# Optimization experiments

Measured on AMD Instinct MI355X. Metric: run time of the kernel, lower is better.

The kernel has to match this reference:

```python
import jax, jax.numpy as jnp
import numpy as np

THRESHOLD = 0.05   # area-ratio cutoff for 'small target'
SMOOTH = 1e-5      # dice smoothing
FG_FRAC = 0.02     # fraction of foreground pixels in synthetic target (< THRESHOLD)


def setup_inputs() -> dict:
    key = jax.random.key(0)
    k1, k2 = jax.random.split(key)
    B, C, H, W = 64, 1, 512, 512
    pred = jax.random.normal(k1, (B, C, H, W), dtype=jnp.float32)
    # sparse binary mask so area_ratio < threshold for (nearly) all samples
    target = (jax.random.uniform(k2, (B, C, H, W)) < FG_FRAC).astype(jnp.float32)
    return {"pred": pred, "target": target}


def reference(pred, target):
    B = pred.shape[0]
    x = pred.reshape(B, -1)    # [B, P] logits
    t = target.reshape(B, -1)  # [B, P] targets in {0,1}

    # per-sample area ratio and validity mask (replaces the Python branch)
    area_ratio = jnp.mean((t > 0.5).astype(jnp.float32), axis=1)  # [B]
    valid = area_ratio < THRESHOLD                                 # [B] bool

    # BCEWithLogits (numerically stable), weighted by clamp(1 + 10*t, max=20)
    bce = jnp.maximum(x, 0.0) - x * t + jnp.log1p(jnp.exp(-jnp.abs(x)))
    pos_weight = jnp.minimum(1.0 + 10.0 * t, 20.0)
    weighted_bce = jnp.mean(bce * pos_weight, axis=1)  # [B]

    # per-sample dice loss
    p = jax.nn.sigmoid(x)
    intersection = jnp.sum(p * t, axis=1)              # [B]
    union = jnp.sum(p, axis=1) + jnp.sum(t, axis=1)    # [B]
    dice_loss = 1.0 - (2.0 * intersection + SMOOTH) / (union + SMOOTH)

    sample_loss = 0.6 * weighted_bce + 0.4 * dice_loss  # [B]

    n_valid = jnp.sum(valid.astype(jnp.float32))
    total = jnp.sum(jnp.where(valid, sample_loss, 0.0))
    return jnp.where(n_valid > 0, total / jnp.maximum(n_valid, 1.0), 0.0)
```

## Files before the change

### kernel.cpp

```cpp
#include <hip/hip_runtime.h>


#define B_SAMPLES 64
#define P_ELEMS   262144
#define P4        (P_ELEMS / 4)
#define BPS       32
#define TPB       256
#define CHUNK4    (P4 / BPS)
#define ITERS     (CHUNK4 / TPB)

__global__ __launch_bounds__(TPB) void stal_partial(
        const float* __restrict__ pred,
        const float* __restrict__ target,
        float* __restrict__ ws) {
    const int blk    = blockIdx.x;
    const int sample = blk >> 5;
    const int bin    = blk & (BPS - 1);
    const int tid    = threadIdx.x;

    const float4* p4 = reinterpret_cast<const float4*>(pred)
                       + (size_t)sample * P4 + (size_t)bin * CHUNK4;
    const float4* t4 = reinterpret_cast<const float4*>(target)
                       + (size_t)sample * P4 + (size_t)bin * CHUNK4;

    float s_bce = 0.f, s_pt = 0.f, s_p = 0.f, s_t = 0.f;

    #pragma unroll
    for (int i = 0; i < ITERS; ++i) {
        float4 xv = p4[tid + i * TPB];
        float4 tv = t4[tid + i * TPB];
        #pragma unroll
        for (int j = 0; j < 4; ++j) {
            float x = (&xv.x)[j];
            float t = (&tv.x)[j];
            float ax = fabsf(x);
            float e  = __expf(-ax);
            float r  = __builtin_amdgcn_rcpf(1.f + e);
            float p  = (x >= 0.f) ? r : 1.f - r;
            float bce = fmaxf(x, 0.f) - x * t + __logf(1.f + e);
            s_bce = fmaf(bce, fmaf(10.f, t, 1.f), s_bce);
            s_p  += p;
            s_pt  = fmaf(p, t, s_pt);
            s_t  += t;
        }
    }

    for (int off = 32; off > 0; off >>= 1) {
        s_bce += __shfl_down(s_bce, off);
        s_pt  += __shfl_down(s_pt,  off);
        s_p   += __shfl_down(s_p,   off);
        s_t   += __shfl_down(s_t,   off);
    }

    __shared__ float red[4][4];
    const int wave = tid >> 6;
    const int lane = tid & 63;
    if (lane == 0) {
        red[wave][0] = s_bce; red[wave][1] = s_pt;
        red[wave][2] = s_p;   red[wave][3] = s_t;
    }
    __syncthreads();
    if (tid == 0) {
        float a = 0.f, b = 0.f, c = 0.f, d = 0.f;
        for (int w = 0; w < 4; ++w) {
            a += red[w][0]; b += red[w][1]; c += red[w][2]; d += red[w][3];
        }
        float* o = ws + (size_t)blk * 4;
        o[0] = a; o[1] = b; o[2] = c; o[3] = d;
    }
}

__global__ __launch_bounds__(64) void stal_finalize(
        const float* __restrict__ ws,
        float* __restrict__ out) {
    const int b = threadIdx.x;

    float S0 = 0.f, S1 = 0.f, S2 = 0.f, S3 = 0.f;
    for (int k = 0; k < BPS; ++k) {
        const float* o = ws + ((size_t)b * BPS + k) * 4;
        S0 += o[0]; S1 += o[1]; S2 += o[2]; S3 += o[3];
    }

    const float invP = 1.f / (float)P_ELEMS;
    float area   = S3 * invP;
    bool  valid  = area < 0.05f;
    float wbce   = S0 * invP;
    float dice   = 1.f - (2.f * S1 + 1e-5f) / (S2 + S3 + 1e-5f);
    float loss   = 0.6f * wbce + 0.4f * dice;

    float v       = valid ? 1.f : 0.f;
    float contrib = valid ? loss : 0.f;
    for (int off = 32; off > 0; off >>= 1) {
        contrib += __shfl_down(contrib, off);
        v       += __shfl_down(v, off);
    }
    if (b == 0) {
        out[0] = (v > 0.f) ? contrib / fmaxf(v, 1.f) : 0.f;
    }
}

extern "C" void kernel_launch(void* const* d_in, const int* in_sizes, int n_in,
                              void* d_out, int out_size, void* d_ws, size_t ws_size,
                              hipStream_t stream) {
    const float* pred   = (const float*)d_in[0];
    const float* target = (const float*)d_in[1];
    float* out = (float*)d_out;
    float* ws  = (float*)d_ws;

    stal_partial <<<B_SAMPLES * BPS, TPB, 0, stream>>>(pred, target, ws);
    stal_finalize<<<1, 64, 0, stream>>>(ws, out);
}
```

Before: 29.24 us.

## Fuse finalize into partial kernel via last-block atomic and simplify BCE math

Merges the two-kernel reduction into one kernel: each block bumps an atomic counter after writing its partials, and the last block to arrive performs the per-sample finalize and the cross-sample mean. The per-element math is also rewritten to use log(1+exp(x)) with an exp2/log2 pair, and the x*t term is pulled out into a separate accumulator, which removes the abs, select and max operations. A memset is added to reset the counter on every call. Because log2(1+exp(x)) is computed without the stable abs form, it can overflow for large positive logits.

Result: slower. 94.66 us (+223.8%).

```diff
diff --git a/kernel.cpp b/kernel.cpp
--- a/kernel.cpp
+++ b/kernel.cpp
@@ -5,14 +5,20 @@
 #define P_ELEMS   262144
 #define P4        (P_ELEMS / 4)
 #define BPS       32
+#define NBLK      (B_SAMPLES * BPS)
 #define TPB       256
 #define CHUNK4    (P4 / BPS)
 #define ITERS     (CHUNK4 / TPB)
 
-__global__ __launch_bounds__(TPB) void stal_partial(
+#define LOG2E 1.44269504088896340736f
+#define LN2   0.69314718055994530942f
+
+__global__ __launch_bounds__(TPB) void stal_fused(
         const float* __restrict__ pred,
         const float* __restrict__ target,
-        float* __restrict__ ws) {
+        float* __restrict__ ws,
+        unsigned int* __restrict__ counter,
+        float* __restrict__ out) {
     const int blk    = blockIdx.x;
     const int sample = blk >> 5;
     const int bin    = blk & (BPS - 1);
@@ -23,7 +29,7 @@
     const float4* t4 = reinterpret_cast<const float4*>(target)
                        + (size_t)sample * P4 + (size_t)bin * CHUNK4;
 
-    float s_bce = 0.f, s_pt = 0.f, s_p = 0.f, s_t = 0.f;
+    float s_l2w = 0.f, s_xt = 0.f, s_p = 0.f, s_pt = 0.f, s_t = 0.f;
 
     #pragma unroll
     for (int i = 0; i < ITERS; ++i) {
@@ -33,17 +39,21 @@
         for (int j = 0; j < 4; ++j) {
             float x = (&xv.x)[j];
             float t = (&tv.x)[j];
-            float ax = fabsf(x);
-            float e  = __expf(-ax);
-            float r  = __builtin_amdgcn_rcpf(1.f + e);
-            float p  = (x >= 0.f) ? r : 1.f - r;
-            float bce = fmaxf(x, 0.f) - x * t + __logf(1.f + e);
-            s_bce = fmaf(bce, fmaf(10.f, t, 1.f), s_bce);
+            float u  = __builtin_amdgcn_exp2f(x * LOG2E);
+            float a  = 1.f + u;
+            float r  = __builtin_amdgcn_rcpf(a);
+            float p  = u * r;
+            float l2 = __log2f(a);
+            float w  = fmaf(10.f, t, 1.f);
+            s_l2w = fmaf(l2, w, s_l2w);
+            s_xt  = fmaf(x,  t, s_xt);
             s_p  += p;
             s_pt  = fmaf(p, t, s_pt);
             s_t  += t;
         }
     }
+
+    float s_bce = fmaf(LN2, s_l2w, -11.f * s_xt);
 
     for (int off = 32; off > 0; off >>= 1) {
         s_bce += __shfl_down(s_bce, off);
@@ -53,6 +63,7 @@
     }
 
     __shared__ float red[4][4];
+    __shared__ int   is_last;
     const int wave = tid >> 6;
     const int lane = tid & 63;
     if (lane == 0) {
@@ -67,35 +78,37 @@
         }
         float* o = ws + (size_t)blk * 4;
         o[0] = a; o[1] = b; o[2] = c; o[3] = d;
+        __threadfence();
+        is_last = (atomicAdd(counter, 1u) == NBLK - 1) ? 1 : 0;
     }
-}
+    __syncthreads();
+    if (!is_last) return;
 
-__global__ __launch_bounds__(64) void stal_finalize(
-        const float* __restrict__ ws,
-        float* __restrict__ out) {
-    const int b = threadIdx.x;
+    __threadfence();
+    if (tid < B_SAMPLES) {
+        const int b = tid;
+        float S0 = 0.f, S1 = 0.f, S2 = 0.f, S3 = 0.f;
+        const float4* w4 = reinterpret_cast<const float4*>(ws) + (size_t)b * BPS;
+        for (int k = 0; k < BPS; ++k) {
+            float4 o = w4[k];
+            S0 += o.x; S1 += o.y; S2 += o.z; S3 += o.w;
+        }
+        const float invP = 1.f / (float)P_ELEMS;
+        float area  = S3 * invP;
+        bool  valid = area < 0.05f;
+        float wbce  = S0 * invP;
+        float dice  = 1.f - (2.f * S1 + 1e-5f) / (S2 + S3 + 1e-5f);
+        float loss  = 0.6f * wbce + 0.4f * dice;
 
-    float S0 = 0.f, S1 = 0.f, S2 = 0.f, S3 = 0.f;
-    for (int k = 0; k < BPS; ++k) {
-        const float* o = ws + ((size_t)b * BPS + k) * 4;
-        S0 += o[0]; S1 += o[1]; S2 += o[2]; S3 += o[3];
-    }
-
-    const float invP = 1.f / (float)P_ELEMS;
-    float area   = S3 * invP;
-    bool  valid  = area < 0.05f;
-    float wbce   = S0 * invP;
-    float dice   = 1.f - (2.f * S1 + 1e-5f) / (S2 + S3 + 1e-5f);
-    float loss   = 0.6f * wbce + 0.4f * dice;
-
-    float v       = valid ? 1.f : 0.f;
-    float contrib = valid ? loss : 0.f;
-    for (int off = 32; off > 0; off >>= 1) {
-        contrib += __shfl_down(contrib, off);
-        v       += __shfl_down(v, off);
-    }
-    if (b == 0) {
-        out[0] = (v > 0.f) ? contrib / fmaxf(v, 1.f) : 0.f;
+        float v       = valid ? 1.f : 0.f;
+        float contrib = valid ? loss : 0.f;
+        for (int off = 32; off > 0; off >>= 1) {
+            contrib += __shfl_down(contrib, off);
+            v       += __shfl_down(v, off);
+        }
+        if (b == 0) {
+            out[0] = (v > 0.f) ? contrib / fmaxf(v, 1.f) : 0.f;
+        }
     }
 }
 
@@ -106,7 +119,8 @@
     const float* target = (const float*)d_in[1];
     float* out = (float*)d_out;
     float* ws  = (float*)d_ws;
+    unsigned int* counter = (unsigned int*)((char*)d_ws + NBLK * 4 * sizeof(float));
 
-    stal_partial <<<B_SAMPLES * BPS, TPB, 0, stream>>>(pred, target, ws);
-    stal_finalize<<<1, 64, 0, stream>>>(ws, out);
+    (void)hipMemsetAsync(counter, 0, sizeof(unsigned int), stream);
+    stal_fused<<<NBLK, TPB, 0, stream>>>(pred, target, ws, counter, out);
 }
```
